# Kernel tuning notes

Measured on AMD Instinct MI355X. Metric: run time of the kernel, lower is better.

Reference implementation:

```python
import jax, jax.numpy as jnp
import numpy as np

IN_CH = 1280
NUM_HEADS = 8
DIM_DOWN = 5
CUT_RATE = 4
SCALE = (IN_CH // NUM_HEADS) ** -0.5  # faithful to original: uses in_ch//num_heads


def setup_inputs() -> dict:
    key = jax.random.key(0)
    ks = jax.random.split(key, 5)
    B, N = 4, 4096
    C = IN_CH // DIM_DOWN  # 256
    x = jax.random.normal(ks[0], (B, N, IN_CH), dtype=jnp.float32)
    Wd = jax.random.normal(ks[1], (IN_CH, C), dtype=jnp.float32) * (IN_CH ** -0.5)
    Wqkv = jax.random.normal(ks[2], (C, 3 * C), dtype=jnp.float32) * (C ** -0.5)
    Wup = jax.random.normal(ks[3], (C, IN_CH), dtype=jnp.float32) * (C ** -0.5)
    bup = jnp.zeros((IN_CH,), dtype=jnp.float32)
    return {"x": x, "Wd": Wd, "Wqkv": Wqkv, "Wup": Wup, "bup": bup}


def reference(x, Wd, Wqkv, Wup, bup):
    # dim-down projection (dropout is identity at rate 0 / eval)
    h = x @ Wd                                  # [B, N, C]
    B, N, C = h.shape
    H = NUM_HEADS
    hd = C // H
    blk = N // CUT_RATE
    qkv = (h @ Wqkv).reshape(B, N, 3, H, hd)
    qkv = jnp.transpose(qkv, (2, 0, 3, 1, 4))   # [3, B, H, N, hd]
    q, k, v = qkv[0], qkv[1], qkv[2]
    # block-diagonal local attention: split N into CUT_RATE independent chunks
    q = q.reshape(B, H, CUT_RATE, blk, hd)
    k = k.reshape(B, H, CUT_RATE, blk, hd)
    v = v.reshape(B, H, CUT_RATE, blk, hd)
    attn = jnp.einsum('bhcqd,bhckd->bhcqk', q, k) * SCALE
    attn = jax.nn.softmax(attn, axis=-1)
    o = jnp.einsum('bhcqk,bhckd->bhcqd', attn, v)
    # torch cat over chunks along token dim, then merge heads: [B, N, C]
    o = jnp.transpose(o, (0, 2, 3, 1, 4)).reshape(B, N, C)
    return o @ Wup + bup
```

## Files before the change

### kernel.cpp

```cpp
#include <hip/hip_runtime.h>

typedef unsigned short u16;
typedef unsigned int u32;
typedef u16 u16x4 __attribute__((ext_vector_type(4)));
typedef u16 u16x8 __attribute__((ext_vector_type(8)));
typedef __bf16 bf16x8 __attribute__((ext_vector_type(8)));
typedef float f32x4 __attribute__((ext_vector_type(4)));

__device__ __forceinline__ u16 f2bf(float f) {
  union { float f; unsigned u; } c; c.f = f;
  unsigned u = c.u;
  return (u16)((u + 0x7fff + ((u >> 16) & 1)) >> 16);
}

__device__ __forceinline__ float fexp2(float x) {
  float r; asm("v_exp_f32 %0, %1" : "=v"(r) : "v"(x)); return r;
}

__device__ __forceinline__ u32 cvtpk(float lo, float hi) {
  u32 r;
  asm("v_cvt_pk_bf16_f32 %0, %1, %2" : "=v"(r) : "v"(lo), "v"(hi));
  return r;
}

__device__ __forceinline__ void lds16(const u16* g, u16* l) {
  __builtin_amdgcn_global_load_lds(
      (const __attribute__((address_space(1))) unsigned int*)g,
      (__attribute__((address_space(3))) unsigned int*)l, 16, 0, 0);
}

#define CEXP (0.07905694150420949f * 1.4426950408889634f)

#define BAR()  do { asm volatile("" ::: "memory"); \
                    __builtin_amdgcn_s_barrier(); \
                    asm volatile("" ::: "memory"); } while (0)
#define VMC(n) asm volatile("s_waitcnt vmcnt(" #n ")" ::: "memory")

#define PREP_W (1280 * 256 + 768 * 256 + 1280 * 256)

__global__ __launch_bounds__(256)
void prep_all(const float* __restrict__ Wd, const float* __restrict__ Wqkv,
              const float* __restrict__ Wup, const float* __restrict__ X,
              u16* __restrict__ WdC, u16* __restrict__ WqkvT,
              u16* __restrict__ WupT, u16* __restrict__ Xb, int n8) {
  int id = blockIdx.x * 256 + threadIdx.x;
  if (id < 1280 * 256) {
    WdC[id] = f2bf(Wd[id]);
    return;
  }
  id -= 1280 * 256;
  if (id < 768 * 256) {
    int n = id >> 8, c = id & 255;
    float v = Wqkv[(size_t)c * 768 + n];
    if (n < 256) v *= CEXP;
    WqkvT[id] = f2bf(v);
    return;
  }
  id -= 768 * 256;
  if (id < 1280 * 256) {
    int n = id >> 8, c = id & 255;
    WupT[id] = f2bf(Wup[(size_t)c * 1280 + n]);
    return;
  }
  id -= 1280 * 256;
  if (id < n8) {
    const float4* src = (const float4*)(X + (size_t)id * 8);
    float4 lo = src[0], hi = src[1];
    u16x8 v;
    v[0]=f2bf(lo.x); v[1]=f2bf(lo.y); v[2]=f2bf(lo.z); v[3]=f2bf(lo.w);
    v[4]=f2bf(hi.x); v[5]=f2bf(hi.y); v[6]=f2bf(hi.z); v[7]=f2bf(hi.w);
    *(u16x8*)(Xb + (size_t)id * 8) = v;
  }
}

template <int AF32>
__global__ __launch_bounds__(256)
void gemm_bt(const void* __restrict__ Av,
             const u16* __restrict__ BT,
             u16* __restrict__ Cb, float* __restrict__ Cf,
             const float* __restrict__ bias,
             int M, int N, int K)
{
  __shared__ u16 As[128][64];
  __shared__ u16 Bs[128][64];
  const int tid  = threadIdx.x;
  const int wave = tid >> 6, lane = tid & 63;
  const int quad = lane >> 4, l16 = lane & 15;
  const int rsw  = l16 & 7;
  const int ssw  = ((lane & 7) ^ (lane >> 3)) << 3;

  const int nb = N >> 7, mb = M >> 7;
  int band, nblk;
  if ((mb & 7) == 0) {
    int xcd = blockIdx.x & 7, slot = blockIdx.x >> 3;
    band = xcd + 8 * (slot / nb);
    nblk = slot % nb;
  } else {
    band = blockIdx.x / nb;
    nblk = blockIdx.x % nb;
  }
  const int m0 = band * 128, n0 = nblk * 128;
  const int wr = (wave >> 1) * 64, wc = (wave & 1) * 64;
  const u16*   A16 = (const u16*)Av;
  const float* A32 = (const float*)Av;

  f32x4 acc[4][4];
#pragma unroll
  for (int i = 0; i < 4; i++)
#pragma unroll
    for (int j = 0; j < 4; j++) acc[i][j] = f32x4{0.f, 0.f, 0.f, 0.f};

  for (int k0 = 0; k0 < K; k0 += 64) {
    if constexpr (AF32) {
#pragma unroll
      for (int it = 0; it < 4; it++) {
        int idx = tid + it * 256;
        int r = idx >> 3;
        const float* src = &A32[(size_t)(m0 + r) * K + k0 + ((idx & 7) << 3)];
        float4 lo = *(const float4*)src;
        float4 hi = *(const float4*)(src + 4);
        u16x8 v;
        v[0]=f2bf(lo.x); v[1]=f2bf(lo.y); v[2]=f2bf(lo.z); v[3]=f2bf(lo.w);
        v[4]=f2bf(hi.x); v[5]=f2bf(hi.y); v[6]=f2bf(hi.z); v[7]=f2bf(hi.w);
        *(u16x8*)&As[r][((idx & 7) ^ (r & 7)) << 3] = v;
      }
#pragma unroll
      for (int it = 0; it < 4; it++) {
        int r0 = wave * 32 + it * 8;
        lds16(&BT[(size_t)(n0 + r0 + (lane >> 3)) * K + k0 + ssw],
              &Bs[r0][0] + lane * 8);
      }
    } else {
#pragma unroll
      for (int it = 0; it < 4; it++) {
        int r0 = wave * 32 + it * 8;
        lds16(&A16[(size_t)(m0 + r0 + (lane >> 3)) * K + k0 + ssw],
              &As[r0][0] + lane * 8);
        lds16(&BT[(size_t)(n0 + r0 + (lane >> 3)) * K + k0 + ssw],
              &Bs[r0][0] + lane * 8);
      }
    }
    __syncthreads();
#pragma unroll
    for (int ks = 0; ks < 64; ks += 32) {
      bf16x8 af[4], bfr[4];
#pragma unroll
      for (int i = 0; i < 4; i++)
        af[i] = *(const bf16x8*)&As[wr + i * 16 + l16][(((ks >> 3) + quad) ^ rsw) << 3];
#pragma unroll
      for (int j = 0; j < 4; j++)
        bfr[j] = *(const bf16x8*)&Bs[wc + j * 16 + l16][(((ks >> 3) + quad) ^ rsw) << 3];
#pragma unroll
      for (int i = 0; i < 4; i++)
#pragma unroll
        for (int j = 0; j < 4; j++)
          acc[i][j] = __builtin_amdgcn_mfma_f32_16x16x32_bf16(af[i], bfr[j], acc[i][j], 0, 0, 0);
    }
    __syncthreads();
  }

#pragma unroll
  for (int i = 0; i < 4; i++) {
#pragma unroll
    for (int j = 0; j < 4; j++) {
      int col = n0 + wc + j * 16 + l16;
      float bv = bias ? bias[col] : 0.0f;
#pragma unroll
      for (int r = 0; r < 4; r++) {
        int row = m0 + wr + i * 16 + quad * 4 + r;
        float v = acc[i][j][r] + bv;
        if (Cf) Cf[(size_t)row * N + col] = v;
        else    Cb[(size_t)row * N + col] = f2bf(v);
      }
    }
  }
}

#define LDA_(d, ib) { _Pragma("unroll") for (int i = 0; i < 4; i++) \
  _Pragma("unroll") for (int ks = 0; ks < 2; ks++) \
    af[i*2+ks] = *(const bf16x8*)&As[d][wm][(ib+i)*16 + l16][((ks*4+quad) ^ rsw) << 3]; }

#define LDB_(d, dst, jp) { _Pragma("unroll") for (int j = 0; j < 2; j++) \
  _Pragma("unroll") for (int ks = 0; ks < 2; ks++) \
    dst[j*2+ks] = *(const bf16x8*)&Bs[d][bh][br + (jp*2+j)*16 + l16][((ks*4+quad) ^ rsw) << 3]; }

#define MM_(ib, jp, breg) { __builtin_amdgcn_s_setprio(1); \
  _Pragma("unroll") for (int i = 0; i < 4; i++) \
  _Pragma("unroll") for (int j = 0; j < 2; j++) \
  _Pragma("unroll") for (int ks = 0; ks < 2; ks++) \
    acc[ib+i][jp*2+j] = __builtin_amdgcn_mfma_f32_16x16x32_bf16( \
        af[i*2+ks], breg[j*2+ks], acc[ib+i][jp*2+j], 0, 0, 0); \
  __builtin_amdgcn_s_setprio(0); }

__global__ __launch_bounds__(512, 2)
void gemm_bt256(const u16* __restrict__ A16, const u16* __restrict__ BT,
                u16* __restrict__ Cb, int M, int N, int K)
{
  __shared__ __align__(16) u16 As[2][2][128][64];
  __shared__ __align__(16) u16 Bs[2][2][128][64];
  const int tid  = threadIdx.x;
  const int wave = tid >> 6, lane = tid & 63;
  const int quad = lane >> 4, l16 = lane & 15;
  const int wm = wave >> 2, wn = wave & 3;
  const int bh = wn >> 1, br = (wn & 1) * 64;
  const int rsw = l16 & 7;

  const int nb = N >> 8, mb = M >> 8;
  int band, nblk;
  if ((mb & 7) == 0) {
    int xcd = blockIdx.x & 7, slot = blockIdx.x >> 3;
    band = xcd + 8 * (slot / nb);
    nblk = slot % nb;
  } else {
    band = blockIdx.x / nb;
    nblk = blockIdx.x % nb;
  }
  const int m0 = band * 256, n0 = nblk * 256;
  const int NT = K >> 6;

  const int srow = tid >> 3;
  const int scol = ((tid & 7) ^ (srow & 7)) << 3;

  auto stageA = [&](int t, int h) {
    const int d = t & 1;
    const size_t g = (size_t)(m0 + h * 128 + srow) * K + (t << 6) + scol;
    lds16(&A16[g], &As[d][h][0][0] + tid * 8);
    lds16(&A16[g + (size_t)64 * K], &As[d][h][64][0] + tid * 8);
  };
  auto stageB = [&](int t, int h) {
    const int d = t & 1;
    const size_t g = (size_t)(n0 + h * 128 + srow) * K + (t << 6) + scol;
    lds16(&BT[g], &Bs[d][h][0][0] + tid * 8);
    lds16(&BT[g + (size_t)64 * K], &Bs[d][h][64][0] + tid * 8);
  };

  bf16x8 af[8], b0[4], b1[4];
  f32x4 acc[8][4];
#pragma unroll
  for (int i = 0; i < 8; i++)
#pragma unroll
    for (int j = 0; j < 4; j++) acc[i][j] = f32x4{0.f, 0.f, 0.f, 0.f};

  stageA(0, 0); stageA(0, 1); stageB(0, 0); stageB(0, 1); stageA(1, 0);
  VMC(2);
  BAR();

  const int nIter = NT >> 1;
  for (int it = 0; it < nIter; ++it) {
    const int t0 = it * 2, t1 = t0 + 1;
    const bool more  = (t0 + 2 < NT);
    const bool more1 = (t1 + 2 < NT);

    LDA_(0, 0); LDB_(0, b0, 0);
    stageA(t1, 1);
    BAR(); MM_(0, 0, b0); BAR();
    LDB_(0, b1, 1);
    stageB(t1, 0);
    BAR(); MM_(0, 1, b1); BAR();
    LDA_(0, 4);
    stageB(t1, 1);
    BAR(); MM_(4, 1, b1); BAR();
    if (more) stageA(t0 + 2, 0);
    BAR(); MM_(4, 0, b0);
    if (more) { VMC(2); } else { VMC(0); }
    BAR();

    LDA_(1, 0); LDB_(1, b0, 0);
    if (more) stageA(t0 + 2, 1);
    BAR(); MM_(0, 0, b0); BAR();
    LDB_(1, b1, 1);
    if (more) stageB(t0 + 2, 0);
    BAR(); MM_(0, 1, b1); BAR();
    LDA_(1, 4);
    if (more) stageB(t0 + 2, 1);
    BAR(); MM_(4, 1, b1); BAR();
    if (more1) stageA(t1 + 2, 0);
    BAR(); MM_(4, 0, b0);
    if (it + 1 < nIter) {
      if (more1) { VMC(2); } else { VMC(0); }
      BAR();
    }
  }

#pragma unroll
  for (int i = 0; i < 8; i++) {
#pragma unroll
    for (int j = 0; j < 4; j++) {
      const int col = n0 + wn * 64 + j * 16 + l16;
#pragma unroll
      for (int r = 0; r < 4; r++) {
        const int row = m0 + wm * 128 + i * 16 + quad * 4 + r;
        Cb[(size_t)row * N + col] = f2bf(acc[i][j][r]);
      }
    }
  }
}

__global__ __launch_bounds__(256)
void vtrans(const u16* __restrict__ qkv, u16* __restrict__ vT)
{
  __shared__ u16 T[32][72];
  const int tid   = threadIdx.x;
  const int kt    = blockIdx.x;
  const int head  = blockIdx.y >> 2;
  const int chunk = blockIdx.y & 3;
  const int b     = blockIdx.z;
  const size_t rowbase = (size_t)b * 4096 + chunk * 1024 + kt * 64;

  const int tok = tid >> 2;
  const int d8  = (tid & 3) << 3;
  u16x8 vv = *(const u16x8*)&qkv[(rowbase + tok) * 768 + 512 + head * 32 + d8];
  const int rot = (tok + (d8 >> 3)) & 7;
#pragma unroll
  for (int jj = 0; jj < 8; jj++) {
    int j = (jj + rot) & 7;
    T[d8 + j][tok] = vv[j];
  }
  __syncthreads();
  const int d = tid >> 3;
  const int s = tid & 7;
  const int base = ((s >> 2) << 5) + ((s & 3) << 2);
  u16x4 lo = *(const u16x4*)&T[d][base];
  u16x4 hi = *(const u16x4*)&T[d][base + 16];
  u16x8 o8;
  o8[0]=lo[0]; o8[1]=lo[1]; o8[2]=lo[2]; o8[3]=lo[3];
  o8[4]=hi[0]; o8[5]=hi[1]; o8[6]=hi[2]; o8[7]=hi[3];
  size_t obase = ((size_t)((b * 4 + chunk) * 8 + head)) * 32768
               + (size_t)d * 1024 + kt * 64 + s * 8;
  *(u16x8*)&vT[obase] = o8;
}

__global__ __launch_bounds__(256)
void attn_kernel(const u16* __restrict__ qkv, const u16* __restrict__ vT,
                 u16* __restrict__ o)
{
  __shared__ __align__(16) u16 Ks[4][64][32];
  __shared__ __align__(16) u16 VTs[4][32][64];

  const int tid  = threadIdx.x;
  const int wave = tid >> 6, lane = tid & 63;
  const int quad = lane >> 4, l16 = lane & 15;
  const int qb    = blockIdx.x;
  const int head  = blockIdx.y >> 2;
  const int chunk = blockIdx.y & 3;
  const int b     = blockIdx.z;
  const size_t rowbase = (size_t)b * 4096 + chunk * 1024;
  const int tok0 = qb * 128 + wave * 32;

  const int kkey = tid >> 2;
  const int kd8  = (tid & 3) << 3;
  const int vr   = tid >> 3;
  const int vs   = tid & 7;
  const int vsl  = (vs ^ (vr & 7)) << 3;
  const size_t vbase = ((size_t)((b * 4 + chunk) * 8 + head)) * 32768
                     + (size_t)vr * 1024 + vsl;

  auto stageKV = [&](int kb, int buf) {
    lds16(&qkv[(rowbase + kb * 64 + kkey) * 768 + 256 + head * 32 + kd8],
          &Ks[buf][0][0] + tid * 8);
    lds16(&vT[vbase + (size_t)kb * 64], &VTs[buf][0][0] + tid * 8);
  };

  stageKV(0, 0);

  bf16x8 qf[2];
#pragma unroll
  for (int qt = 0; qt < 2; qt++)
    qf[qt] = *(const bf16x8*)&qkv[(rowbase + tok0 + qt * 16 + l16) * 768 + head * 32 + quad * 8];

  stageKV(1, 1);

  bf16x8 onesb;
  {
    union { u16x8 u; bf16x8 v; } c;
#pragma unroll
    for (int i = 0; i < 8; i++) c.u[i] = 0x3F80;
    onesb = c.v;
  }

  f32x4 Oacc[2][2], Osum[2];
#pragma unroll
  for (int qt = 0; qt < 2; qt++) {
    Osum[qt] = f32x4{0.f, 0.f, 0.f, 0.f};
#pragma unroll
    for (int nd = 0; nd < 2; nd++) Oacc[qt][nd] = f32x4{0.f, 0.f, 0.f, 0.f};
  }

  VMC(2);
  BAR();

  for (int kb = 0; kb < 16; kb++) {
    const int cur = kb & 3;
    if (kb + 2 < 16) stageKV(kb + 2, (kb + 2) & 3);

    bf16x8 kf[4];
#pragma unroll
    for (int kt = 0; kt < 4; kt++)
      kf[kt] = *(const bf16x8*)&Ks[cur][kt * 16 + l16][quad * 8];

    f32x4 ST[4][2];
    __builtin_amdgcn_s_setprio(1);
#pragma unroll
    for (int kt = 0; kt < 4; kt++)
#pragma unroll
      for (int qt = 0; qt < 2; qt++)
        ST[kt][qt] = __builtin_amdgcn_mfma_f32_16x16x32_bf16(kf[kt], qf[qt], f32x4{0.f,0.f,0.f,0.f}, 0, 0, 0);
    __builtin_amdgcn_s_setprio(0);

    u32 pw[2][4][2];
#pragma unroll
    for (int qt = 0; qt < 2; qt++)
#pragma unroll
      for (int kt = 0; kt < 4; kt++) {
        float p0 = fexp2(ST[kt][qt][0]);
        float p1 = fexp2(ST[kt][qt][1]);
        float p2 = fexp2(ST[kt][qt][2]);
        float p3 = fexp2(ST[kt][qt][3]);
        pw[qt][kt][0] = cvtpk(p0, p1);
        pw[qt][kt][1] = cvtpk(p2, p3);
      }

#pragma unroll
    for (int ks = 0; ks < 2; ks++) {
      bf16x8 vf[2];
#pragma unroll
      for (int nd = 0; nd < 2; nd++)
        vf[nd] = *(const bf16x8*)&VTs[cur][nd * 16 + l16][((ks * 4 + quad) ^ (l16 & 7)) << 3];
      __builtin_amdgcn_s_setprio(1);
#pragma unroll
      for (int qt = 0; qt < 2; qt++) {
        union { u32 w[4]; bf16x8 v; } pu;
        pu.w[0] = pw[qt][2 * ks][0];
        pu.w[1] = pw[qt][2 * ks][1];
        pu.w[2] = pw[qt][2 * ks + 1][0];
        pu.w[3] = pw[qt][2 * ks + 1][1];
#pragma unroll
        for (int nd = 0; nd < 2; nd++)
          Oacc[qt][nd] = __builtin_amdgcn_mfma_f32_16x16x32_bf16(pu.v, vf[nd], Oacc[qt][nd], 0, 0, 0);
        Osum[qt] = __builtin_amdgcn_mfma_f32_16x16x32_bf16(pu.v, onesb, Osum[qt], 0, 0, 0);
      }
      __builtin_amdgcn_s_setprio(0);
    }

    if (kb < 15) {
      if (kb + 2 < 16) { VMC(2); } else { VMC(0); }
      BAR();
    }
  }

#pragma unroll
  for (int qt = 0; qt < 2; qt++)
#pragma unroll
    for (int r = 0; r < 4; r++) {
      float inv = 1.0f / Osum[qt][r];
      size_t row = rowbase + tok0 + qt * 16 + quad * 4 + r;
#pragma unroll
      for (int nd = 0; nd < 2; nd++) {
        int col = head * 32 + nd * 16 + l16;
        o[row * 256 + col] = f2bf(Oacc[qt][nd][r] * inv);
      }
    }
}

extern "C" void kernel_launch(void* const* d_in, const int* in_sizes, int n_in,
                              void* d_out, int out_size, void* d_ws, size_t ws_size,
                              hipStream_t stream)
{
  const float* x    = (const float*)d_in[0];
  const float* Wd   = (const float*)d_in[1];
  const float* Wqkv = (const float*)d_in[2];
  const float* Wup  = (const float*)d_in[3];
  const float* bup  = (const float*)d_in[4];
  float* out = (float*)d_out;

  const int M = 4 * 4096;

  u16* WdC   = (u16*)d_ws;
  u16* WqkvT = WdC   + 1280 * 256;
  u16* WupT  = WqkvT + 768 * 256;
  u16* WpT   = WupT  + 1280 * 256;
  u16* qkv   = WpT   + 768 * 1280;
  u16* ob    = qkv   + (size_t)M * 768;
  u16* xb    = ob    + (size_t)M * 256;
  u16* vT    = xb;

  const size_t need = ((size_t)(1280*256 + 768*256 + 1280*256 + 768*1280)
                       + (size_t)M * (768 + 256 + 1280)) * sizeof(u16);
  const bool use_xb = ws_size >= need;

  const int n8 = use_xb ? (M * 1280 / 8) : 0;
  prep_all<<<(PREP_W + n8 + 255) / 256, 256, 0, stream>>>(
      Wd, Wqkv, Wup, x, WdC, WqkvT, WupT, xb, n8);

  gemm_bt<0><<<dim3((1280 / 128) * (768 / 128)), 256, 0, stream>>>(
      (const void*)WqkvT, WdC, WpT, nullptr, nullptr, 768, 1280, 256);

  if (use_xb) {
    gemm_bt256<<<dim3((768 / 256) * (M / 256)), 512, 0, stream>>>(
        xb, WpT, qkv, M, 768, 1280);
  } else {
    gemm_bt<1><<<dim3((768 / 128) * (M / 128)), 256, 0, stream>>>(
        (const void*)x, WpT, qkv, nullptr, nullptr, M, 768, 1280);
  }

  vtrans<<<dim3(16, 32, 4), 256, 0, stream>>>(qkv, vT);

  attn_kernel<<<dim3(8, 32, 4), 256, 0, stream>>>(qkv, vT, ob);

  gemm_bt<0><<<dim3((1280 / 128) * (M / 128)), 256, 0, stream>>>(
      (const void*)ob, WupT, nullptr, out, bup, M, 1280, 256);
}
```

Baseline: 273.9 us.

## Overlap weight-product GEMM with x bf16 cast and reorder attention grid

```diff
diff --git a/kernel.cpp b/kernel.cpp
--- a/kernel.cpp
+++ b/kernel.cpp
@@ -39,10 +39,10 @@
 #define PREP_W (1280 * 256 + 768 * 256 + 1280 * 256)
 
 __global__ __launch_bounds__(256)
-void prep_all(const float* __restrict__ Wd, const float* __restrict__ Wqkv,
-              const float* __restrict__ Wup, const float* __restrict__ X,
-              u16* __restrict__ WdC, u16* __restrict__ WqkvT,
-              u16* __restrict__ WupT, u16* __restrict__ Xb, int n8) {
+void prep_w(const float* __restrict__ Wd, const float* __restrict__ Wqkv,
+            const float* __restrict__ Wup,
+            u16* __restrict__ WdC, u16* __restrict__ WqkvT,
+            u16* __restrict__ WupT) {
   int id = blockIdx.x * 256 + threadIdx.x;
   if (id < 1280 * 256) {
     WdC[id] = f2bf(Wd[id]);
@@ -60,17 +60,85 @@
   if (id < 1280 * 256) {
     int n = id >> 8, c = id & 255;
     WupT[id] = f2bf(Wup[(size_t)c * 1280 + n]);
+  }
+}
+
+__global__ __launch_bounds__(256)
+void wpt_xcast(const u16* __restrict__ WqkvT, const u16* __restrict__ WdC,
+               u16* __restrict__ WpT,
+               const float* __restrict__ X, u16* __restrict__ Xb, int n8)
+{
+  __shared__ u16 As[128][64];
+  __shared__ u16 Bs[128][64];
+
+  if (blockIdx.x >= 60) {
+    int id = (blockIdx.x - 60) * 256 + threadIdx.x;
+    if (id < n8) {
+      const float4* src = (const float4*)(X + (size_t)id * 8);
+      float4 lo = src[0], hi = src[1];
+      u16x8 v;
+      v[0]=f2bf(lo.x); v[1]=f2bf(lo.y); v[2]=f2bf(lo.z); v[3]=f2bf(lo.w);
+      v[4]=f2bf(hi.x); v[5]=f2bf(hi.y); v[6]=f2bf(hi.z); v[7]=f2bf(hi.w);
+      *(u16x8*)(Xb + (size_t)id * 8) = v;
+    }
     return;
   }
-  id -= 1280 * 256;
-  if (id < n8) {
-    const float4* src = (const float4*)(X + (size_t)id * 8);
-    float4 lo = src[0], hi = src[1];
-    u16x8 v;
-    v[0]=f2bf(lo.x); v[1]=f2bf(lo.y); v[2]=f2bf(lo.z); v[3]=f2bf(lo.w);
-    v[4]=f2bf(hi.x); v[5]=f2bf(hi.y); v[6]=f2bf(hi.z); v[7]=f2bf(hi.w);
-    *(u16x8*)(Xb + (size_t)id * 8) = v;
-  }
+
+  const int tid  = threadIdx.x;
+  const int wave = tid >> 6, lane = tid & 63;
+  const int quad = lane >> 4, l16 = lane & 15;
+  const int rsw  = l16 & 7;
+  const int ssw  = ((lane & 7) ^ (lane >> 3)) << 3;
+  const int band = blockIdx.x / 10, nblk = blockIdx.x % 10;
+  const int m0 = band * 128, n0 = nblk * 128;
+  const int wr = (wave >> 1) * 64, wc = (wave & 1) * 64;
+  const int K = 256, N = 1280;
+
+  f32x4 acc[4][4];
+#pragma unroll
+  for (int i = 0; i < 4; i++)
+#pragma unroll
+    for (int j = 0; j < 4; j++) acc[i][j] = f32x4{0.f, 0.f, 0.f, 0.f};
+
+  for (int k0 = 0; k0 < K; k0 += 64) {
+#pragma unroll
+    for (int it = 0; it < 4; it++) {
+      int r0 = wave * 32 + it * 8;
+      lds16(&WqkvT[(size_t)(m0 + r0 + (lane >> 3)) * K + k0 + ssw],
+            &As[r0][0] + lane * 8);
+      lds16(&WdC[(size_t)(n0 + r0 + (lane >> 3)) * K + k0 + ssw],
+            &Bs[r0][0] + lane * 8);
+    }
+    __syncthreads();
+#pragma unroll
+    for (int ks = 0; ks < 64; ks += 32) {
+      bf16x8 af[4], bfr[4];
+#pragma unroll
+      for (int i = 0; i < 4; i++)
+        af[i] = *(const bf16x8*)&As[wr + i * 16 + l16][(((ks >> 3) + quad) ^ rsw) << 3];
+#pragma unroll
+      for (int j = 0; j < 4; j++)
+        bfr[j] = *(const bf16x8*)&Bs[wc + j * 16 + l16][(((ks >> 3) + quad) ^ rsw) << 3];
+#pragma unroll
+      for (int i = 0; i < 4; i++)
+#pragma unroll
+        for (int j = 0; j < 4; j++)
+          acc[i][j] = __builtin_amdgcn_mfma_f32_16x16x32_bf16(af[i], bfr[j], acc[i][j], 0, 0, 0);
+    }
+    __syncthreads();
+  }
+
+#pragma unroll
+  for (int i = 0; i < 4; i++)
+#pragma unroll
+    for (int j = 0; j < 4; j++) {
+      int col = n0 + wc + j * 16 + l16;
+#pragma unroll
+      for (int r = 0; r < 4; r++) {
+        int row = m0 + wr + i * 16 + quad * 4 + r;
+        WpT[(size_t)row * N + col] = f2bf(acc[i][j][r]);
+      }
+    }
 }
 
 template <int AF32>
@@ -340,10 +408,12 @@
   const int tid  = threadIdx.x;
   const int wave = tid >> 6, lane = tid & 63;
   const int quad = lane >> 4, l16 = lane & 15;
-  const int qb    = blockIdx.x;
-  const int head  = blockIdx.y >> 2;
-  const int chunk = blockIdx.y & 3;
-  const int b     = blockIdx.z;
+  const int gid   = blockIdx.x;
+  const int qb    = gid >> 7;
+  const int g     = gid & 127;
+  const int head  = g >> 4;
+  const int chunk = (g >> 2) & 3;
+  const int b     = g & 3;
   const size_t rowbase = (size_t)b * 4096 + chunk * 1024;
   const int tok0 = qb * 128 + wave * 32;
 
@@ -488,12 +558,12 @@
                        + (size_t)M * (768 + 256 + 1280)) * sizeof(u16);
   const bool use_xb = ws_size >= need;
 
+  prep_w<<<(PREP_W + 255) / 256, 256, 0, stream>>>(
+      Wd, Wqkv, Wup, WdC, WqkvT, WupT);
+
   const int n8 = use_xb ? (M * 1280 / 8) : 0;
-  prep_all<<<(PREP_W + n8 + 255) / 256, 256, 0, stream>>>(
-      Wd, Wqkv, Wup, x, WdC, WqkvT, WupT, xb, n8);
-
-  gemm_bt<0><<<dim3((1280 / 128) * (768 / 128)), 256, 0, stream>>>(
-      (const void*)WqkvT, WdC, WpT, nullptr, nullptr, 768, 1280, 256);
+  wpt_xcast<<<60 + (n8 + 255) / 256, 256, 0, stream>>>(
+      WqkvT, WdC, WpT, x, xb, n8);
 
   if (use_xb) {
     gemm_bt256<<<dim3((768 / 256) * (M / 256)), 512, 0, stream>>>(
@@ -505,7 +575,7 @@
 
   vtrans<<<dim3(16, 32, 4), 256, 0, stream>>>(qkv, vT);
 
-  attn_kernel<<<dim3(8, 32, 4), 256, 0, stream>>>(qkv, vT, ob);
+  attn_kernel<<<dim3(1024), 256, 0, stream>>>(qkv, vT, ob);
 
   gemm_bt<0><<<dim3((1280 / 128) * (M / 128)), 256, 0, stream>>>(
       (const void*)ob, WupT, nullptr, out, bup, M, 1280, 256);
```

Result: faster. 259.8 us (-5.2%).
